# Kernel optimization log

Hardware: AMD Instinct MI355X
Metric: run time of the kernel (lower is better)

The kernel has to match this reference:

```python
import jax, jax.numpy as jnp
import numpy as np

B, S, D, H = 4, 2048, 512, 8
INNER = D  # assumed AttentionHead.inner_size == size (naive single-head attention)


def setup_inputs() -> dict:
    key = jax.random.key(0)
    ks = jax.random.split(key, 8)
    scale = 0.02
    return {
        "emb_input": jax.random.normal(ks[0], (B, S, D), dtype=jnp.float32),
        "Wq": jax.random.normal(ks[1], (H, D, INNER), dtype=jnp.float32) * scale,
        "bq": jnp.zeros((H, INNER), dtype=jnp.float32),
        "Wk": jax.random.normal(ks[2], (H, D, INNER), dtype=jnp.float32) * scale,
        "bk": jnp.zeros((H, INNER), dtype=jnp.float32),
        "Wv": jax.random.normal(ks[3], (H, D, INNER), dtype=jnp.float32) * scale,
        "bv": jnp.zeros((H, INNER), dtype=jnp.float32),
        "Wp": jax.random.normal(ks[4], (H * INNER, D), dtype=jnp.float32) * scale,
        "bp": jnp.zeros((D,), dtype=jnp.float32),
    }


def reference(emb_input, Wq, bq, Wk, bk, Wv, bv, Wp, bp):
    # All heads batched into one einsum instead of a Python loop over submodules.
    x = emb_input  # [B, S, D]
    q = jnp.einsum("bsd,hde->bhse", x, Wq) + bq[None, :, None, :]  # [B,H,S,E]
    k = jnp.einsum("bsd,hde->bhse", x, Wk) + bk[None, :, None, :]
    v = jnp.einsum("bsd,hde->bhse", x, Wv) + bv[None, :, None, :]
    scores = jnp.einsum("bhse,bhte->bhst", q, k) / jnp.sqrt(
        jnp.asarray(INNER, dtype=x.dtype)
    )  # [B,H,S,S]
    attn = jax.nn.softmax(scores, axis=-1)
    o = jnp.einsum("bhst,bhte->bhse", attn, v)  # [B,H,S,E]
    # concat over heads (dim=2 in torch => feature dim after per-head outputs)
    o = jnp.transpose(o, (0, 2, 1, 3)).reshape(B, S, H * INNER)
    return o @ Wp + bp  # [B, S, D]
```

## Files before the change

kernel.cpp:

```cpp
#include <hip/hip_runtime.h>


typedef short s8v __attribute__((ext_vector_type(8)));
typedef float f4v __attribute__((ext_vector_type(4)));
typedef unsigned short us;
typedef us us4v __attribute__((ext_vector_type(4)));

__device__ inline us f2b(float f) {
  union { float f; unsigned u; } v; v.f = f;
  unsigned r = v.u + 0x7FFFu + ((v.u >> 16) & 1u);
  return (us)(r >> 16);
}

__device__ inline void gld16(const us* g, us* l) {
  __builtin_amdgcn_global_load_lds(
      (const __attribute__((address_space(1))) void*)g,
      (__attribute__((address_space(3))) void*)l, 16, 0, 0);
}

template <int EPI>
__global__ __launch_bounds__(512, 2) void gemm_nt(
    const us* __restrict__ A, int lda, long long sA0, long long sA1,
    const us* __restrict__ Bm, int ldb, long long sB0, long long sB1,
    const float* __restrict__ bias, const float* __restrict__ bias2,
    const float* __restrict__ bias3,
    void* __restrict__ Cv, void* __restrict__ C2, void* __restrict__ C3,
    int ldc, long long sC0, long long sC1,
    int K, float alpha, int L, int sbits) {
  __shared__ __align__(16) us As[2][16384];
  __shared__ __align__(16) us Bs[2][16384];
  const int t = threadIdx.x;
  const int wv = t >> 6, ln = t & 63;
  const int m16 = ln & 15, quad = ln >> 4;

  const int gx = gridDim.x, gxy = gx * gridDim.y;
  const int nblk = gxy * gridDim.z;
  const int flat = blockIdx.x + gx * blockIdx.y + gxy * blockIdx.z;
  int nid = flat;
  if ((nblk & 7) == 0) nid = (flat & 7) * (nblk >> 3) + (flat >> 3);
  const int bz = nid / gxy, rem = nid % gxy;
  const int by = rem / gx, bx = rem % gx;

  const long long row0 = (long long)by * 256;
  const long long col0 = (long long)bx * 256;
  const int zo = bz >> L, zi = bz & ((1 << L) - 1);
  const us* Az = A + zo * sA0 + zi * sA1;
  const us* Bz = Bm + zo * sB0 + zi * sB1;

  int offA[4], offB[4];
#pragma unroll
  for (int j = 0; j < 4; ++j) {
    const int c = t + 512 * j;
    const int s = c >> 6, l = c & 63;
    const int mb = s >> 1, ks = s & 1, qd = (l >> 4) & 3, mm = l & 15;
    offA[j] = (int)((row0 + mb * 16 + mm) * (long long)lda + ks * 32 + qd * 8);
    offB[j] = (int)((col0 + mb * 16 + mm) * (long long)ldb + ks * 32 + qd * 8);
  }

  f4v acc[8][4];
#pragma unroll
  for (int r = 0; r < 8; ++r)
#pragma unroll
    for (int c = 0; c < 4; ++c) acc[r][c] = (f4v){0.f, 0.f, 0.f, 0.f};

  const int nk = K >> 6;
  const int wr = wv >> 2, wc = wv & 3;

#define STAGE(kt2, bb)                                                        \
  {                                                                           \
    const int kof = (kt2) << 6;                                               \
    _Pragma("unroll") for (int j = 0; j < 4; ++j)                             \
        gld16(Az + offA[j] + kof, (us*)As[bb] + (t + 512 * j) * 8);           \
    _Pragma("unroll") for (int j = 0; j < 4; ++j)                             \
        gld16(Bz + offB[j] + kof, (us*)Bs[bb] + (t + 512 * j) * 8);           \
  }

  STAGE(0, 0);
  STAGE(1, 1);

  for (int kt = 0; kt < nk; ++kt) {
    const int b = kt & 1;
    if (kt + 1 < nk)
      asm volatile("s_waitcnt vmcnt(8)" ::: "memory");
    else
      asm volatile("s_waitcnt vmcnt(0)" ::: "memory");
    __builtin_amdgcn_s_barrier();

    s8v bfr[8];
#pragma unroll
    for (int c = 0; c < 4; ++c)
#pragma unroll
      for (int ks = 0; ks < 2; ++ks)
        bfr[c * 2 + ks] =
            *(const s8v*)&Bs[b][(((wc * 4 + c) * 2 + ks) * 64 + ln) * 8];

#pragma unroll
    for (int p = 0; p < 4; ++p) {
      s8v af[4];
#pragma unroll
      for (int rr = 0; rr < 2; ++rr)
#pragma unroll
        for (int ks = 0; ks < 2; ++ks)
          af[rr * 2 + ks] = *(const s8v*)&As[b]
              [(((wr * 8 + p * 2 + rr) * 2 + ks) * 64 + ln) * 8];
      __builtin_amdgcn_s_barrier();
      asm volatile("s_waitcnt lgkmcnt(0)" ::: "memory");
      __builtin_amdgcn_sched_barrier(0);
      __builtin_amdgcn_s_setprio(1);
#pragma unroll
      for (int ks = 0; ks < 2; ++ks)
#pragma unroll
        for (int rr = 0; rr < 2; ++rr)
#pragma unroll
          for (int c = 0; c < 4; ++c)
            acc[p * 2 + rr][c] = __builtin_amdgcn_mfma_f32_16x16x32_bf16(
                af[rr * 2 + ks], bfr[c * 2 + ks], acc[p * 2 + rr][c], 0, 0, 0);
      __builtin_amdgcn_s_setprio(0);
      __builtin_amdgcn_s_barrier();
    }
    if (kt + 2 < nk) STAGE(kt + 2, b);
  }
#undef STAGE

  if (EPI == 6) {
#pragma unroll
    for (int r = 0; r < 8; ++r)
#pragma unroll
      for (int c = 0; c < 4; ++c)
#pragma unroll
        for (int g = 0; g < 4; ++g)
          acc[r][c][g] = __expf(fmaf(acc[r][c][g], alpha, -4.f));
  }
#pragma unroll
  for (int r = 0; r < 8; ++r) {
    const int inRow = wr * 128 + r * 16 + quad * 4;
    const long long gr0 = row0 + inRow;
#pragma unroll
    for (int c = 0; c < 4; ++c) {
      const long long gc = col0 + wc * 64 + c * 16 + m16;
      if (EPI == 3) {
        const int which = (int)(gc >> sbits);
        const int gsec = (int)gc & ((1 << sbits) - 1);
        const int hc = gsec >> 9, e = (int)gc & 511;
        const long long slice =
            ((long long)zo * (1 << (sbits - 9)) + hc) * 1048576LL;
        if (which == 0) {
          us* C = (us*)Cv;
          const float bb = bias[gsec];
#pragma unroll
          for (int g = 0; g < 4; ++g)
            C[slice + (gr0 + g) * 512 + e] = f2b(acc[r][c][g] + bb);
        } else if (which == 1) {
          us* C = (us*)C2;
          const float bb = bias2[gsec];
#pragma unroll
          for (int g = 0; g < 4; ++g)
            C[slice + (gr0 + g) * 512 + e] = f2b(acc[r][c][g] + bb);
        } else {
          us* C = (us*)C3;
          const float bb = bias3[gsec];
          us4v pk;
#pragma unroll
          for (int g = 0; g < 4; ++g) pk[g] = f2b(acc[r][c][g] + bb);
          *(us4v*)&C[slice + (long long)e * 2048 + gr0] = pk;
        }
      } else if (EPI == 5) {
        float* C = (float*)Cv + zo * sC0;
        float* p = C + gr0 * ldc + gc;
#pragma unroll
        for (int g = 0; g < 4; ++g)
          atomicAdd(&p[(long long)g * ldc], acc[r][c][g] * alpha);
      } else if (EPI == 6) {
        us* C = (us*)Cv + zo * sC0 + zi * sC1;
#pragma unroll
        for (int g = 0; g < 4; ++g)
          C[(gr0 + g) * (long long)ldc + gc] = f2b(acc[r][c][g]);
      } else {
        us* C = (us*)Cv + zo * sC0 + zi * sC1;
        const float* lrow = (const float*)C2 + (long long)bz * 2048;
#pragma unroll
        for (int g = 0; g < 4; ++g) {
          const float inv = 1.f / lrow[gr0 + g];
          C[(gr0 + g) * (long long)ldc + gc] = f2b(acc[r][c][g] * inv);
        }
      }
    }
    if (EPI == 6) {
      float* lsum = (float*)C2 + (long long)bz * 2048;
#pragma unroll
      for (int g = 0; g < 4; ++g) {
        float s = acc[r][0][g] + acc[r][1][g] + acc[r][2][g] + acc[r][3][g];
        s += __shfl_xor(s, 1, 64);
        s += __shfl_xor(s, 2, 64);
        s += __shfl_xor(s, 4, 64);
        s += __shfl_xor(s, 8, 64);
        if (m16 == 0) atomicAdd(&lsum[gr0 + g], s);
      }
    }
  }
}

__global__ __launch_bounds__(256) void conv_bf16(const float* __restrict__ in,
                                                 us* __restrict__ out, int n4) {
  const int i = blockIdx.x * 256 + threadIdx.x;
  if (i < n4) {
    const float4 f = ((const float4*)in)[i];
    us4v o;
    o[0] = f2b(f.x); o[1] = f2b(f.y); o[2] = f2b(f.z); o[3] = f2b(f.w);
    ((us4v*)out)[i] = o;
  }
}

__global__ __launch_bounds__(256) void conv_transpose(const float* __restrict__ in,
                                                      us* __restrict__ out,
                                                      int R, int C, int Lc,
                                                      int mask, long long sChunk) {
  __shared__ float tile[32][33];
  const int tx = threadIdx.x & 31, ty = threadIdx.x >> 5;
  const int z = blockIdx.z;
  const long long zi = (long long)z * R * C;
  us* dst = out + (long long)(z >> Lc) * sChunk + (long long)(z & mask) * R * C;
  const int r0 = blockIdx.y * 32, c0 = blockIdx.x * 32;
#pragma unroll
  for (int j = 0; j < 4; ++j)
    tile[ty + 8 * j][tx] = in[zi + (long long)(r0 + ty + 8 * j) * C + c0 + tx];
  __syncthreads();
#pragma unroll
  for (int j = 0; j < 4; ++j)
    dst[(long long)(c0 + ty + 8 * j) * R + r0 + tx] = f2b(tile[tx][ty + 8 * j]);
}

__global__ __launch_bounds__(256) void init_out_kernel(float* __restrict__ out,
                                                       const float* __restrict__ bp,
                                                       int total,
                                                       float* __restrict__ lz,
                                                       int lcnt) {
  const int i = blockIdx.x * 256 + threadIdx.x;
  if (i < total) out[i] = bp[i & 511];
  else if (i < total + lcnt) lz[i - total] = 0.f;
}

extern "C" void kernel_launch(void* const* d_in, const int* in_sizes, int n_in,
                              void* d_out, int out_size, void* d_ws, size_t ws_size,
                              hipStream_t stream) {
  constexpr int Bb = 4, S = 2048, D = 512, H = 8, E = 512, HE = 4096;
  const float* x  = (const float*)d_in[0];
  const float* Wq = (const float*)d_in[1];
  const float* bq = (const float*)d_in[2];
  const float* Wk = (const float*)d_in[3];
  const float* bk = (const float*)d_in[4];
  const float* Wv = (const float*)d_in[5];
  const float* bv = (const float*)d_in[6];
  const float* Wp = (const float*)d_in[7];
  const float* bp = (const float*)d_in[8];
  float* out = (float*)d_out;

  const long long SE = (long long)S * E, SS = (long long)S * S;
  const long long SD = (long long)S * D, ED = (long long)E * D;

  us* xh  = (us*)d_ws;
  us* W3  = xh + 4194304;
  us* WpT = W3 + 6291456;
  us* dyn = WpT + 2097152;

  const size_t fixedB = (size_t)(4194304 + 6291456 + 2097152) * 2;
  const size_t lB = (size_t)H * Bb * S * 4;
  int HC = 8;
  while (HC > 1) {
    const size_t need = fixedB + lB +
        (size_t)HC * (3 * (size_t)Bb * SE + (size_t)Bb * SS) * 2;
    if (need <= ws_size) break;
    HC >>= 1;
  }
  const int Lh = (HC == 8) ? 3 : (HC == 4) ? 2 : (HC == 2) ? 1 : 0;
  const int BHC = Bb * HC;
  const int sbits = 9 + Lh;

  us* qh = dyn;
  us* kh = qh + (size_t)BHC * SE;
  us* vT = kh + (size_t)BHC * SE;
  us* sc = vT + (size_t)BHC * SE;
  float* lb = (float*)(sc + (size_t)BHC * SS);
  us* oh = qh;

  const dim3 tb(256), tg(512);
  const int lcnt = H * Bb * S;
  init_out_kernel<<<dim3((Bb * S * D + lcnt + 255) / 256), tb, 0, stream>>>(
      out, bp, Bb * S * D, lb, lcnt);
  conv_bf16<<<dim3(4194304 / 4 / 256), tb, 0, stream>>>(x, xh, 4194304 / 4);
  const long long sChunk = 3LL * HC * ED;
  conv_transpose<<<dim3(16, 16, H), tb, 0, stream>>>(Wq, W3, D, E, Lh, HC - 1, sChunk);
  conv_transpose<<<dim3(16, 16, H), tb, 0, stream>>>(Wk, W3 + HC * ED, D, E, Lh, HC - 1, sChunk);
  conv_transpose<<<dim3(16, 16, H), tb, 0, stream>>>(Wv, W3 + 2 * HC * ED, D, E, Lh, HC - 1, sChunk);
  conv_transpose<<<dim3(16, 128, 1), tb, 0, stream>>>(Wp, WpT, HE, D, 0, 0, 0);

  const float aS = 0.044194173824159216f;
  const dim3 gQKV(3 * HC * E / 256, 8, Bb);
  const dim3 gS(8, 8, BHC);
  const dim3 gPV(2, 8, BHC);
  const dim3 gOP(2, 8, BHC);

  for (int c = 0; c < H / HC; ++c) {
    const int h0 = c * HC;
    float* lc = lb + (long long)c * BHC * S;
    gemm_nt<3><<<gQKV, tg, 0, stream>>>(
        xh, D, SD, 0, W3 + c * sChunk, D, 0, 0,
        bq + h0 * E, bk + h0 * E, bv + h0 * E,
        qh, kh, vT, 512, 0, SE, D, 1.f, 0, sbits);
    gemm_nt<6><<<gS, tg, 0, stream>>>(
        qh, E, (long long)HC * SE, SE, kh, E, (long long)HC * SE, SE,
        nullptr, nullptr, nullptr, sc, lc, nullptr,
        S, (long long)HC * SS, SS, E, aS, Lh, 0);
    gemm_nt<7><<<gPV, tg, 0, stream>>>(
        sc, S, (long long)HC * SS, SS, vT, S, (long long)HC * SE, SE,
        nullptr, nullptr, nullptr, oh, lc, nullptr,
        HC * E, (long long)S * HC * E, E, S, 1.f, Lh, 0);
    gemm_nt<5><<<gOP, tg, 0, stream>>>(
        oh, HC * E, (long long)S * HC * E, 512,
        WpT + (long long)h0 * E, HE, 0, 512,
        nullptr, nullptr, nullptr, out, nullptr, nullptr,
        D, SD, 0, 512, 1.f, Lh, 0);
  }
}
```

Before: 1.046 ms.

## Interleave split global-to-LDS prefetches across the MFMA sub-phases of the GEMM loop

Replaces the single bulk prefetch at the end of each k-iteration with smaller global_load_lds batches spread across the four MFMA quarter-phases. Each batch is issued only once the LDS region it overwrites has been read, with B and A halves scheduled separately. The end-of-iteration wait becomes vmcnt(6). The aim is to overlap memory traffic more evenly with MFMA work and shorten the stall at the top of each iteration. The cost is a more intricate wait and barrier protocol that relies on exact counter accounting.

```diff
diff --git a/kernel.cpp b/kernel.cpp
--- a/kernel.cpp
+++ b/kernel.cpp
@@ -66,61 +66,84 @@
   const int nk = K >> 6;
   const int wr = wv >> 2, wc = wv & 3;
 
-#define STAGE(kt2, bb)                                                        \
-  {                                                                           \
-    const int kof = (kt2) << 6;                                               \
-    _Pragma("unroll") for (int j = 0; j < 4; ++j)                             \
-        gld16(Az + offA[j] + kof, (us*)As[bb] + (t + 512 * j) * 8);           \
-    _Pragma("unroll") for (int j = 0; j < 4; ++j)                             \
-        gld16(Bz + offB[j] + kof, (us*)Bs[bb] + (t + 512 * j) * 8);           \
-  }
-
-  STAGE(0, 0);
-  STAGE(1, 1);
+#define BARR __builtin_amdgcn_s_barrier()
+#define LGKM0                                              \
+  do {                                                     \
+    asm volatile("s_waitcnt lgkmcnt(0)" ::: "memory");     \
+    __builtin_amdgcn_sched_barrier(0);                     \
+  } while (0)
+#define READ_A(p_)                                                           \
+  _Pragma("unroll") for (int rr = 0; rr < 2; ++rr)                           \
+  _Pragma("unroll") for (int ks = 0; ks < 2; ++ks)                           \
+      af[rr * 2 + ks] = *(const s8v*)&As[b]                                  \
+          [(((wr * 8 + (p_) * 2 + rr) * 2 + ks) * 64 + ln) * 8];
+#define MFMA_Q(p_)                                                           \
+  __builtin_amdgcn_s_setprio(1);                                             \
+  _Pragma("unroll") for (int ks = 0; ks < 2; ++ks)                           \
+  _Pragma("unroll") for (int rr = 0; rr < 2; ++rr)                           \
+  _Pragma("unroll") for (int c = 0; c < 4; ++c)                              \
+      acc[(p_) * 2 + rr][c] = __builtin_amdgcn_mfma_f32_16x16x32_bf16(       \
+          af[rr * 2 + ks], bfr[c * 2 + ks], acc[(p_) * 2 + rr][c], 0, 0, 0); \
+  __builtin_amdgcn_s_setprio(0);
+
+#pragma unroll
+  for (int j = 0; j < 4; ++j) gld16(Az + offA[j], (us*)As[0] + (t + 512 * j) * 8);
+#pragma unroll
+  for (int j = 0; j < 4; ++j) gld16(Bz + offB[j], (us*)Bs[0] + (t + 512 * j) * 8);
+  if (nk > 1) {
+#pragma unroll
+    for (int j = 0; j < 4; ++j)
+      gld16(Bz + offB[j] + 64, (us*)Bs[1] + (t + 512 * j) * 8);
+    gld16(Az + offA[0] + 64, (us*)As[1] + t * 8);
+    gld16(Az + offA[2] + 64, (us*)As[1] + (t + 1024) * 8);
+    asm volatile("s_waitcnt vmcnt(6)" ::: "memory");
+  } else {
+    asm volatile("s_waitcnt vmcnt(0)" ::: "memory");
+  }
+  BARR;
 
   for (int kt = 0; kt < nk; ++kt) {
     const int b = kt & 1;
-    if (kt + 1 < nk)
-      asm volatile("s_waitcnt vmcnt(8)" ::: "memory");
-    else
-      asm volatile("s_waitcnt vmcnt(0)" ::: "memory");
-    __builtin_amdgcn_s_barrier();
-
-    s8v bfr[8];
+    s8v bfr[8], af[4];
 #pragma unroll
     for (int c = 0; c < 4; ++c)
 #pragma unroll
       for (int ks = 0; ks < 2; ++ks)
         bfr[c * 2 + ks] =
             *(const s8v*)&Bs[b][(((wc * 4 + c) * 2 + ks) * 64 + ln) * 8];
-
-#pragma unroll
-    for (int p = 0; p < 4; ++p) {
-      s8v af[4];
-#pragma unroll
-      for (int rr = 0; rr < 2; ++rr)
-#pragma unroll
-        for (int ks = 0; ks < 2; ++ks)
-          af[rr * 2 + ks] = *(const s8v*)&As[b]
-              [(((wr * 8 + p * 2 + rr) * 2 + ks) * 64 + ln) * 8];
-      __builtin_amdgcn_s_barrier();
-      asm volatile("s_waitcnt lgkmcnt(0)" ::: "memory");
-      __builtin_amdgcn_sched_barrier(0);
-      __builtin_amdgcn_s_setprio(1);
-#pragma unroll
-      for (int ks = 0; ks < 2; ++ks)
-#pragma unroll
-        for (int rr = 0; rr < 2; ++rr)
-#pragma unroll
-          for (int c = 0; c < 4; ++c)
-            acc[p * 2 + rr][c] = __builtin_amdgcn_mfma_f32_16x16x32_bf16(
-                af[rr * 2 + ks], bfr[c * 2 + ks], acc[p * 2 + rr][c], 0, 0, 0);
-      __builtin_amdgcn_s_setprio(0);
-      __builtin_amdgcn_s_barrier();
-    }
-    if (kt + 2 < nk) STAGE(kt + 2, b);
-  }
-#undef STAGE
+    READ_A(0);
+    if (kt + 1 < nk) {
+      const int kof = (kt + 1) << 6;
+      gld16(Az + offA[1] + kof, (us*)As[b ^ 1] + (t + 512) * 8);
+      gld16(Az + offA[3] + kof, (us*)As[b ^ 1] + (t + 1536) * 8);
+    }
+    asm volatile("s_waitcnt lgkmcnt(8)" ::: "memory");
+    BARR; LGKM0; MFMA_Q(0); BARR;
+    READ_A(1);
+    if (kt + 2 < nk) {
+      const int kof = (kt + 2) << 6;
+#pragma unroll
+      for (int j = 0; j < 4; ++j)
+        gld16(Bz + offB[j] + kof, (us*)Bs[b] + (t + 512 * j) * 8);
+    }
+    BARR; LGKM0; MFMA_Q(1); BARR;
+    READ_A(2);
+    if (kt + 2 < nk) {
+      const int kof = (kt + 2) << 6;
+      gld16(Az + offA[0] + kof, (us*)As[b] + t * 8);
+      gld16(Az + offA[2] + kof, (us*)As[b] + (t + 1024) * 8);
+    }
+    BARR; LGKM0; MFMA_Q(2); BARR;
+    READ_A(3);
+    BARR; LGKM0; MFMA_Q(3);
+    if (kt + 2 < nk) asm volatile("s_waitcnt vmcnt(6)" ::: "memory");
+    else             asm volatile("s_waitcnt vmcnt(0)" ::: "memory");
+    BARR;
+  }
+#undef READ_A
+#undef MFMA_Q
+#undef BARR
+#undef LGKM0
 
   if (EPI == 6) {
 #pragma unroll
```

New measurement: 935.2 us, median of 2. 1.12x faster.
